# Kernel tuning notes

Measured on AMD Instinct MI355X. Metric: run time of the kernel, lower is better.

The kernel has to match this reference:

```python
import jax, jax.numpy as jnp
import numpy as np

SEQ_LEN = 512
D_MODEL = 512
N_HEADS = 8
KERNEL = 7
E_DIM = D_MODEL // N_HEADS  # d_values = 64
PAD = KERNEL // 2


def _gen_D(L):
    D = np.zeros((L - 1, L), dtype=np.float32)
    D[:, 1:] += np.eye(L - 1, dtype=np.float32)
    D[:, :-1] -= np.eye(L - 1, dtype=np.float32)
    return D


def setup_inputs() -> dict:
    key = jax.random.key(0)
    k1, k2, k3 = jax.random.split(key, 3)
    B = 16
    values = jax.random.normal(k1, (B, SEQ_LEN, N_HEADS, E_DIM), dtype=jnp.float32)
    # second-order difference operator, then SVD of D^T D (as in __init__)
    D = _gen_D(SEQ_LEN - 1) @ _gen_D(SEQ_LEN)          # (L-2, L)
    U_np, S_np, _ = np.linalg.svd(D.T @ D)             # (L, L), (L,)
    U = jnp.asarray(U_np, dtype=jnp.float32)
    S = jnp.asarray(S_np, dtype=jnp.float32)
    # Conv1d(E, 1, kernel) parameters
    bound = 1.0 / np.sqrt(E_DIM * KERNEL)
    conv_w = jax.random.uniform(k2, (1, E_DIM, KERNEL), minval=-bound, maxval=bound, dtype=jnp.float32)
    conv_b = jax.random.uniform(k3, (1,), minval=-bound, maxval=bound, dtype=jnp.float32)
    return {"values": values, "conv_w": conv_w, "conv_b": conv_b, "U": U, "S": S}


def reference(values, conv_w, conv_b, U, S):
    B, L, H, E = values.shape
    # lambda predictor: conv1d over length with replicate padding, then 1+elu
    x = values.transpose(0, 2, 3, 1).reshape(B * H, E, L)          # (BH, E, L)
    xp = jnp.pad(x, ((0, 0), (0, 0), (PAD, PAD)), mode='edge')
    y = jax.lax.conv_general_dilated(
        xp, conv_w, window_strides=(1,), padding='VALID',
        dimension_numbers=('NCH', 'OIH', 'NCH'))                   # (BH, 1, L)
    y = y + conv_b[None, :, None]
    lambdas = 1.0 + jax.nn.elu(y).reshape(B, H, L).transpose(0, 2, 1)  # (B, L, H)
    # diagonal reweighting in the U basis: U diag(1/(1+lambda*S)) U^T @ values
    inv = 1.0 / (1.0 + jnp.einsum('blh,l->bhl', lambdas, S))       # (B, H, L)
    t = jnp.einsum('jm,bjhd->bhmd', U, values)                      # project onto U columns
    t = t * inv[..., None]                                          # diagonal scale (fused, no LxL diag)
    out = jnp.einsum('im,bhmd->bihd', U, t)                         # (B, L, H, E)
    return out
```

## Files before the change

### kernel.cpp

```cpp
#include <hip/hip_runtime.h>
#include <hip/hip_bf16.h>
#include <cstdint>
#include <cmath>

#define LSEQ 512
#define EDIM 64
#define NBIG 8192

typedef __attribute__((ext_vector_type(8))) short short8;
typedef __attribute__((ext_vector_type(8))) unsigned short ushort8v;
typedef __attribute__((ext_vector_type(4))) float f32x4;

__device__ __forceinline__ unsigned short f2bf(float f) {
    union { float f; unsigned int u; } x; x.f = f;
    unsigned int r = x.u + 0x7FFFu + ((x.u >> 16) & 1u);
    return (unsigned short)(r >> 16);
}

__device__ __forceinline__ void async_copy16(void* lds, const void* g) {
    auto g1 = (const __attribute__((address_space(1))) void*)g;
    auto l3 = (__attribute__((address_space(3))) void*)lds;
    __builtin_amdgcn_global_load_lds(g1, l3, 16, 0, 0);
}

__device__ __forceinline__ void store16_swz(unsigned short* rowptr, int cbase,
                                            int q, int row,
                                            const unsigned short* o) {
    int x = row & 7, x1 = x >> 1, x0 = x & 1;
    unsigned short* dst = rowptr + cbase + ((q ^ x1) << 4);
    ushort8v lo = *(const ushort8v*)o;
    ushort8v hi = *(const ushort8v*)(o + 8);
    if (x0) { *(ushort8v*)dst = hi; *(ushort8v*)(dst + 8) = lo; }
    else    { *(ushort8v*)dst = lo; *(ushort8v*)(dst + 8) = hi; }
}

__global__ __launch_bounds__(256) void prep_kernel(
        const float* __restrict__ vals, const float* __restrict__ U,
        const float* __restrict__ cw, const float* __restrict__ cb,
        const float* __restrict__ S,
        unsigned short* __restrict__ Vpp, unsigned short* __restrict__ Ut,
        unsigned short* __restrict__ Ub, float* __restrict__ inv) {
    __shared__ float Ls[70 * 65];
    __shared__ float red[16][64];
    __shared__ float wcoef[448];
    int id = blockIdx.x;
    int t = threadIdx.x;

    if (id < 1024) {
        int b = id >> 6, h = (id >> 3) & 7, jt = id & 7;
        int j0 = jt * 64;
        for (int idx = t; idx < 448; idx += 256) wcoef[idx] = cw[idx];
        const float* base = vals + (size_t)b * 262144 + h * 64;
        #pragma unroll
        for (int i = 0; i < 5; ++i) {
            int idx = i * 256 + t;
            if (idx < 1120) {
                int row = idx >> 4, c4 = (idx & 15) * 4;
                int grow = j0 + row - 3;
                grow = grow < 0 ? 0 : (grow > 511 ? 511 : grow);
                float4 v = *(const float4*)(base + (size_t)grow * 512 + c4);
                float* d = &Ls[row * 65 + c4];
                d[0] = v.x; d[1] = v.y; d[2] = v.z; d[3] = v.w;
            }
        }
        __syncthreads();

        {
            int e = t & 63, q = t >> 6;
            unsigned short o[16];
            #pragma unroll
            for (int jj = 0; jj < 16; ++jj)
                o[jj] = f2bf(Ls[(3 + q * 16 + jj) * 65 + e]);
            int n = b * 512 + h * 64 + e;
            store16_swz(Vpp + (size_t)n * 512, j0, q, n, o);
        }

        {
            int lg = t & 15, q16 = t >> 4;
            int l0 = lg * 4, e0 = q16 * 4;
            float rv[10][4];
            #pragma unroll
            for (int r = 0; r < 10; ++r)
                #pragma unroll
                for (int je = 0; je < 4; ++je)
                    rv[r][je] = Ls[(l0 + r) * 65 + e0 + je];
            float a4[4] = {0.f, 0.f, 0.f, 0.f};
            #pragma unroll
            for (int kk = 0; kk < 7; ++kk) {
                #pragma unroll
                for (int je = 0; je < 4; ++je) {
                    float w = wcoef[(e0 + je) * 7 + kk];
                    #pragma unroll
                    for (int dl = 0; dl < 4; ++dl)
                        a4[dl] += rv[dl + kk][je] * w;
                }
            }
            #pragma unroll
            for (int dl = 0; dl < 4; ++dl) red[q16][l0 + dl] = a4[dl];
        }
        __syncthreads();
        if (t < 64) {
            float y = cb[0];
            #pragma unroll
            for (int g = 0; g < 16; ++g) y += red[g][t];
            float lam = (y > 0.f) ? (1.f + y) : expf(y);
            inv[(size_t)(b * 8 + h) * 512 + j0 + t] = 1.f / (1.f + lam * S[j0 + t]);
        }
    } else {
        int id2 = id - 1024;
        int j0 = (id2 >> 3) * 64, m0 = (id2 & 7) * 64;
        int r = t >> 2, q = t & 3;
        int c16 = q * 16;
        float v[16];
        const float* src = U + (size_t)(j0 + r) * 512 + m0 + c16;
        #pragma unroll
        for (int k = 0; k < 16; k += 4) {
            float4 vv = *(const float4*)(src + k);
            v[k] = vv.x; v[k+1] = vv.y; v[k+2] = vv.z; v[k+3] = vv.w;
        }
        {
            unsigned short o[16];
            #pragma unroll
            for (int k = 0; k < 16; ++k) o[k] = f2bf(v[k]);
            store16_swz(Ub + (size_t)(j0 + r) * 512, m0, q, j0 + r, o);
        }
        #pragma unroll
        for (int k = 0; k < 16; ++k) Ls[r * 65 + c16 + k] = v[k];
        __syncthreads();
        {
            unsigned short o[16];
            #pragma unroll
            for (int k = 0; k < 16; ++k) o[k] = f2bf(Ls[(c16 + k) * 65 + r]);
            store16_swz(Ut + (size_t)(m0 + r) * 512, j0, q, m0 + r, o);
        }
    }
}

template<int EPI>
__launch_bounds__(256, 2)
__global__ void gemm_kernel(const unsigned short* __restrict__ A,
                            const unsigned short* __restrict__ B,
                            const float* __restrict__ inv,
                            unsigned short* __restrict__ Tout,
                            float* __restrict__ Out) {
    __shared__ __align__(16) unsigned short As[2][128 * 64];
    __shared__ __align__(16) unsigned short Bs[2][64 * 64];

    int bid = blockIdx.x;
    bid = (bid & 7) * 64 + (bid >> 3);
    int mt = bid & 3, nt = bid >> 2;
    int m0 = mt * 128, n0 = nt * 64;
    int t = threadIdx.x, lane = t & 63, wave = t >> 6;
    int wm = wave >> 1, wn = wave & 1;
    int l15 = lane & 15, l4 = lane >> 4;

    f32x4 acc[4][2] = {};

    const unsigned short* Ab = A + (size_t)(m0 + (t >> 3)) * 512 + (t & 7) * 8;
    const unsigned short* Bb = B + (size_t)(n0 + (t >> 3)) * 512 + (t & 7) * 8;

    auto STAGE = [&](int buf, int kk) {
        int ko = kk * 64;
        unsigned short* ap = &As[buf][t * 8];
        unsigned short* bp = &Bs[buf][t * 8];
        async_copy16(ap,        Ab + ko);
        async_copy16(ap + 2048, Ab + 32 * 512 + ko);
        async_copy16(ap + 4096, Ab + 64 * 512 + ko);
        async_copy16(ap + 6144, Ab + 96 * 512 + ko);
        async_copy16(bp,        Bb + ko);
        async_copy16(bp + 2048, Bb + 32 * 512 + ko);
    };
    auto COMPUTE = [&](int buf) {
        #pragma unroll
        for (int k2 = 0; k2 < 2; ++k2) {
            short8 a[4], bf[2];
            #pragma unroll
            for (int i = 0; i < 4; ++i) {
                int row = wm * 64 + i * 16 + l15;
                a[i] = *(const short8*)&As[buf][row * 64 + (((k2 * 4 + l4) ^ (row & 7)) << 3)];
            }
            #pragma unroll
            for (int j = 0; j < 2; ++j) {
                int row = wn * 32 + j * 16 + l15;
                bf[j] = *(const short8*)&Bs[buf][row * 64 + (((k2 * 4 + l4) ^ (row & 7)) << 3)];
            }
            #pragma unroll
            for (int i = 0; i < 4; ++i)
                #pragma unroll
                for (int j = 0; j < 2; ++j)
                    acc[i][j] = __builtin_amdgcn_mfma_f32_16x16x32_bf16(a[i], bf[j], acc[i][j], 0, 0, 0);
        }
    };

    STAGE(0, 0);
    __syncthreads();
    int cur = 0;
    #pragma unroll
    for (int kk = 0; kk < 7; ++kk) {
        STAGE(cur ^ 1, kk + 1);
        COMPUTE(cur);
        __syncthreads();
        cur ^= 1;
    }
    COMPUTE(cur);

    #pragma unroll
    for (int i = 0; i < 4; ++i) {
        int mb = m0 + wm * 64 + i * 16 + l4 * 4;
        if (EPI == 1) {
            float4 s = *(const float4*)&inv[(size_t)nt * 512 + mb];
            #pragma unroll
            for (int j = 0; j < 2; ++j) {
                int n = n0 + wn * 32 + j * 16 + l15;
                f32x4 v = acc[i][j];
                ushort4 pack;
                pack.x = f2bf(v[0] * s.x);
                pack.y = f2bf(v[1] * s.y);
                pack.z = f2bf(v[2] * s.z);
                pack.w = f2bf(v[3] * s.w);
                int e = mb & 63;
                int pos = (mb & ~63) + ((((e >> 3) ^ (n & 7)) << 3) | (e & 7));
                *(ushort4*)&Tout[(size_t)n * 512 + pos] = pack;
            }
        } else {
            #pragma unroll
            for (int j = 0; j < 2; ++j) {
                int n = n0 + wn * 32 + j * 16 + l15;
                int b = n >> 9, hd = n & 511;
                f32x4 v = acc[i][j];
                float* o = Out + (size_t)b * 262144 + (size_t)mb * 512 + hd;
                o[0] = v[0]; o[512] = v[1]; o[1024] = v[2]; o[1536] = v[3];
            }
        }
    }
}

extern "C" void kernel_launch(void* const* d_in, const int* in_sizes, int n_in,
                              void* d_out, int out_size, void* d_ws, size_t ws_size,
                              hipStream_t stream) {
    const float* vals = (const float*)d_in[0];
    const float* cw   = (const float*)d_in[1];
    const float* cb   = (const float*)d_in[2];
    const float* U    = (const float*)d_in[3];
    const float* S    = (const float*)d_in[4];
    float* out = (float*)d_out;

    const size_t off_Ut  = 0;
    const size_t off_Ub  = 524288;
    const size_t off_V   = 1048576;
    const size_t off_T   = 9437184;
    const size_t off_inv = 17825792;
    const size_t ws_need = 18087936;
    if (ws_size < ws_need) return;

    char* ws = (char*)d_ws;
    unsigned short* Ut  = (unsigned short*)(ws + off_Ut);
    unsigned short* Ub  = (unsigned short*)(ws + off_Ub);
    unsigned short* Vpp = (unsigned short*)(ws + off_V);
    unsigned short* Tpp = (unsigned short*)(ws + off_T);
    float*          inv = (float*)(ws + off_inv);

    prep_kernel<<<1088, 256, 0, stream>>>(vals, U, cw, cb, S, Vpp, Ut, Ub, inv);
    gemm_kernel<1><<<512, 256, 0, stream>>>(Ut, Vpp, inv, Tpp, nullptr);
    gemm_kernel<2><<<512, 256, 0, stream>>>(Ub, Tpp, nullptr, nullptr, out);
}
```

Before: 34.63 us.

## Load GEMM fragments directly from global memory instead of LDS staging

Removes the double-buffered LDS staging (global_load_lds plus barriers) in the GEMM kernel. Each wave now reads its MFMA operand fragments straight from global memory, using the swizzled layout already written by the producer. This drops LDS traffic and synchronisation, but it also drops intra-block operand sharing across waves and leaves latency hiding to the compiler. The result is more global or L2 traffic per block.

```diff
diff --git a/kernel.cpp b/kernel.cpp
--- a/kernel.cpp
+++ b/kernel.cpp
@@ -15,12 +15,6 @@
     union { float f; unsigned int u; } x; x.f = f;
     unsigned int r = x.u + 0x7FFFu + ((x.u >> 16) & 1u);
     return (unsigned short)(r >> 16);
-}
-
-__device__ __forceinline__ void async_copy16(void* lds, const void* g) {
-    auto g1 = (const __attribute__((address_space(1))) void*)g;
-    auto l3 = (__attribute__((address_space(3))) void*)lds;
-    __builtin_amdgcn_global_load_lds(g1, l3, 16, 0, 0);
 }
 
 __device__ __forceinline__ void store16_swz(unsigned short* rowptr, int cbase,
@@ -143,9 +137,6 @@
                             const float* __restrict__ inv,
                             unsigned short* __restrict__ Tout,
                             float* __restrict__ Out) {
-    __shared__ __align__(16) unsigned short As[2][128 * 64];
-    __shared__ __align__(16) unsigned short Bs[2][64 * 64];
-
     int bid = blockIdx.x;
     bid = (bid & 7) * 64 + (bid >> 3);
     int mt = bid & 3, nt = bid >> 2;
@@ -156,53 +147,42 @@
 
     f32x4 acc[4][2] = {};
 
-    const unsigned short* Ab = A + (size_t)(m0 + (t >> 3)) * 512 + (t & 7) * 8;
-    const unsigned short* Bb = B + (size_t)(n0 + (t >> 3)) * 512 + (t & 7) * 8;
-
-    auto STAGE = [&](int buf, int kk) {
-        int ko = kk * 64;
-        unsigned short* ap = &As[buf][t * 8];
-        unsigned short* bp = &Bs[buf][t * 8];
-        async_copy16(ap,        Ab + ko);
-        async_copy16(ap + 2048, Ab + 32 * 512 + ko);
-        async_copy16(ap + 4096, Ab + 64 * 512 + ko);
-        async_copy16(ap + 6144, Ab + 96 * 512 + ko);
-        async_copy16(bp,        Bb + ko);
-        async_copy16(bp + 2048, Bb + 32 * 512 + ko);
-    };
-    auto COMPUTE = [&](int buf) {
+    const unsigned short* abase[4];
+    int ax[4];
+    #pragma unroll
+    for (int i = 0; i < 4; ++i) {
+        int row = m0 + wm * 64 + i * 16 + l15;
+        abase[i] = A + (size_t)row * 512;
+        ax[i] = row & 7;
+    }
+    const unsigned short* bbase[2];
+    int bx[2];
+    #pragma unroll
+    for (int j = 0; j < 2; ++j) {
+        int row = n0 + wn * 32 + j * 16 + l15;
+        bbase[j] = B + (size_t)row * 512;
+        bx[j] = row & 7;
+    }
+
+    #pragma unroll
+    for (int kk = 0; kk < 8; ++kk) {
         #pragma unroll
         for (int k2 = 0; k2 < 2; ++k2) {
-            short8 a[4], bf[2];
-            #pragma unroll
-            for (int i = 0; i < 4; ++i) {
-                int row = wm * 64 + i * 16 + l15;
-                a[i] = *(const short8*)&As[buf][row * 64 + (((k2 * 4 + l4) ^ (row & 7)) << 3)];
-            }
-            #pragma unroll
-            for (int j = 0; j < 2; ++j) {
-                int row = wn * 32 + j * 16 + l15;
-                bf[j] = *(const short8*)&Bs[buf][row * 64 + (((k2 * 4 + l4) ^ (row & 7)) << 3)];
-            }
+            int g = k2 * 4 + l4;
+            short8 a[4], bfr[2];
+            #pragma unroll
+            for (int i = 0; i < 4; ++i)
+                a[i] = *(const short8*)(abase[i] + kk * 64 + ((g ^ ax[i]) << 3));
+            #pragma unroll
+            for (int j = 0; j < 2; ++j)
+                bfr[j] = *(const short8*)(bbase[j] + kk * 64 + ((g ^ bx[j]) << 3));
             #pragma unroll
             for (int i = 0; i < 4; ++i)
                 #pragma unroll
                 for (int j = 0; j < 2; ++j)
-                    acc[i][j] = __builtin_amdgcn_mfma_f32_16x16x32_bf16(a[i], bf[j], acc[i][j], 0, 0, 0);
-        }
-    };
-
-    STAGE(0, 0);
-    __syncthreads();
-    int cur = 0;
-    #pragma unroll
-    for (int kk = 0; kk < 7; ++kk) {
-        STAGE(cur ^ 1, kk + 1);
-        COMPUTE(cur);
-        __syncthreads();
-        cur ^= 1;
-    }
-    COMPUTE(cur);
+                    acc[i][j] = __builtin_amdgcn_mfma_f32_16x16x32_bf16(a[i], bfr[j], acc[i][j], 0, 0, 0);
+        }
+    }
 
     #pragma unroll
     for (int i = 0; i < 4; ++i) {
```

Result: slower. 42.60 us (+23.0%).
